# Kernel optimization log

Hardware: AMD Instinct MI355X
Metric: run time of the kernel (lower is better)

Reference implementation:

```python
import jax, jax.numpy as jnp
import numpy as np


def lstm_encode(x, Wih, Whh, b):
    """x: [S, T, F] -> final hidden state [S, H]. PyTorch LSTM gate order (i, f, g, o)."""
    S = x.shape[0]
    H = Whh.shape[1]

    def step(carry, xt):
        h, c = carry
        z = xt @ Wih.T + h @ Whh.T + b  # [S, 4H]
        i, f, g, o = jnp.split(z, 4, axis=-1)
        c = jax.nn.sigmoid(f) * c + jax.nn.sigmoid(i) * jnp.tanh(g)
        h = jax.nn.sigmoid(o) * jnp.tanh(c)
        return (h, c), None

    init = (jnp.zeros((S, H), x.dtype), jnp.zeros((S, H), x.dtype))
    (h, _), _ = jax.lax.scan(step, init, jnp.swapaxes(x, 0, 1))
    return h


def gatv2(h, Ws, Wd, a, bias):
    """Dense GATv2 on batched fully-connected graphs (no self loops).
    h: [G, N, Hin]; Ws, Wd: [nh, Hin, O]; a: [nh, O]; bias: [nh, O] -> [G, N, nh, O].
    Graph is fully connected (all i != j), so edge-softmax == dense row softmax
    with the diagonal masked out; this is the efficient dense form of the
    gather / LeakyReLU / edge-softmax / scatter pattern in DGL's GATv2Conv."""
    nh = Ws.shape[0]
    N = h.shape[1]
    self_mask = jnp.eye(N, dtype=bool)
    outs = []
    for hd in range(nh):  # small fixed head count; loop caps peak memory
        fs = h @ Ws[hd]  # [G, N, O] source-projected feats (messages)
        fd = h @ Wd[hd]  # [G, N, O] dst-projected feats
        e = jax.nn.leaky_relu(fd[:, :, None, :] + fs[:, None, :, :], 0.2)  # [G, dst, src, O]
        logits = jnp.where(self_mask, -jnp.inf, e @ a[hd])  # [G, dst, src]
        attn = jax.nn.softmax(logits, axis=-1)
        outs.append(jnp.einsum('gds,gso->gdo', attn, fs) + bias[hd])
    return jnp.stack(outs, axis=2)


def cosine(x, y, eps=1e-6):
    xn = x / jnp.maximum(jnp.linalg.norm(x, axis=-1, keepdims=True), eps)
    yn = y / jnp.maximum(jnp.linalg.norm(y, axis=-1, keepdims=True), eps)
    return (xn * yn).sum(-1)


def setup_inputs() -> dict:
    key = jax.random.key(0)
    B, K, T, N, F, H, GH, NH = 16, 4, 64, 128, 16, 32, 32, 8
    ks = jax.random.split(key, 16)

    def rn(k, shape, scale=1.0):
        return jax.random.normal(k, shape, jnp.float32) * scale

    return {
        'anchor': rn(ks[0], (B, T, N, F)),
        'pos': rn(ks[1], (B, T, N, F)),
        'neg': rn(ks[2], (B, K, T, N, F)),
        'hideout': rn(ks[3], (B, 2)),
        'timestep': jax.random.uniform(ks[4], (B, 1), jnp.float32),
        'Wih': rn(ks[5], (4 * H, F), 1.0 / np.sqrt(F)),
        'Whh': rn(ks[6], (4 * H, H), 1.0 / np.sqrt(H)),
        'b_lstm': rn(ks[7], (4 * H,), 0.1),
        'W1s': rn(ks[8], (NH, H, H), 1.0 / np.sqrt(H)),
        'W1d': rn(ks[9], (NH, H, H), 1.0 / np.sqrt(H)),
        'a1': rn(ks[10], (NH, H), 1.0 / np.sqrt(H)),
        'b1': rn(ks[11], (NH, H), 0.1),
        'W2s': rn(ks[12], (1, H, GH), 1.0 / np.sqrt(H)),
        'W2d': rn(ks[13], (1, H, GH), 1.0 / np.sqrt(H)),
        'a2': rn(ks[14], (1, GH), 1.0 / np.sqrt(GH)),
        'b2': rn(ks[15], (1, GH), 0.1),
        'num_agents': 128,
    }


def reference(anchor, pos, neg, hideout, timestep, Wih, Whh, b_lstm,
              W1s, W1d, a1, b1, W2s, W2d, a2, b2, num_agents):
    B, T, N, F = anchor.shape
    K = neg.shape[1]
    H = Whh.shape[1]
    # per-agent time series -> LSTM sequences
    a_seq = jnp.transpose(anchor, (0, 2, 1, 3)).reshape(B * N, T, F)
    p_seq = jnp.transpose(pos, (0, 2, 1, 3)).reshape(B * N, T, F)
    n_seq = jnp.transpose(neg, (0, 1, 3, 2, 4)).reshape(B * K * N, T, F)
    hn = lstm_encode(jnp.concatenate([a_seq, p_seq, n_seq], 0), Wih, Whh, b_lstm)
    hg = hn.reshape(-1, N, H)  # [(2+K)*B, N, H] batched fully-connected graphs
    h1 = gatv2(hg, W1s, W1d, a1, b1).mean(axis=2)  # mean over 8 heads
    h2 = gatv2(h1, W2s, W2d, a2, b2)[:, :, 0, :]   # single head, squeezed
    pooled = h2.mean(axis=1)                        # AvgPooling over nodes
    anchor_res = pooled[:B]
    pos_res = pooled[B:2 * B]
    neg_res = pooled[2 * B:].reshape(B, K, -1)
    sim_pos = cosine(anchor_res, pos_res)[:, None]      # [B, 1]
    sim_neg = cosine(anchor_res[:, None, :], neg_res)   # [B, K]
    all_vecs = jnp.concatenate([sim_neg, sim_pos], axis=1)  # positive last
    contrastive = (-jax.nn.log_softmax(all_vecs, axis=1)[:, -1]).mean()
    res = jnp.concatenate([anchor_res, hideout, timestep], axis=-1)
    return res, contrastive
```

## Files before the change

kernel.cpp:

```cpp
#include <hip/hip_runtime.h>
#include <math.h>


typedef __bf16 bf16x8 __attribute__((ext_vector_type(8)));
typedef float  f32x4  __attribute__((ext_vector_type(4)));
typedef unsigned int u32x4 __attribute__((ext_vector_type(4)));

__device__ __forceinline__ float fast_rcp(float x) { return __builtin_amdgcn_rcpf(x); }
__device__ __forceinline__ float sigm(float x)     { return fast_rcp(1.f + __expf(-x)); }
__device__ __forceinline__ float tanh_fast(float x){ return fmaf(2.f, fast_rcp(1.f + __expf(-2.f * x)), -1.f); }

#define KEEP4(x) asm volatile("" : "+v"(x))

__global__ __launch_bounds__(256, 1) void lstm_mfma_kernel(
    const float* __restrict__ anchor, const float* __restrict__ pos,
    const float* __restrict__ neg, const float* __restrict__ Wih,
    const float* __restrict__ Whh, const float* __restrict__ bias,
    float* __restrict__ hn)
{
    __shared__ unsigned int Hbuf[4][512];
    const int tid  = threadIdx.x;
    const int w    = tid >> 6;
    const int lane = tid & 63;
    const int l15  = lane & 15;
    const int g4   = lane >> 4;
    unsigned int* hb = Hbuf[w];

    #pragma unroll
    for (int i = 0; i < 8; ++i) hb[lane + i * 64] = 0u;

    u32x4 whhH[8], whhL[8], wihH[8];
    float bq[8];
    #pragma unroll
    for (int f = 0; f < 8; ++f) {
        const int G = f >> 1, Hh = f & 1;
        const int c = G * 32 + Hh * 16 + l15;
        bq[f] = bias[c];
        union { u32x4 u; bf16x8 v; } th, tl, ti;
        const float* wr = Whh + c * 32 + g4 * 8;
        #pragma unroll
        for (int i = 0; i < 8; ++i) {
            float wv = wr[i];
            __bf16 hi = (__bf16)wv;
            th.v[i] = hi;
            tl.v[i] = (__bf16)(wv - (float)hi);
        }
        if (g4 < 2) {
            const float* wr2 = Wih + c * 16 + g4 * 8;
            #pragma unroll
            for (int i = 0; i < 8; ++i) ti.v[i] = (__bf16)wr2[i];
        } else {
            #pragma unroll
            for (int i = 0; i < 8; ++i) ti.v[i] = (__bf16)0.f;
        }
        whhH[f] = th.u; whhL[f] = tl.u; wihH[f] = ti.u;
    }
    #pragma unroll
    for (int f = 0; f < 8; ++f) { KEEP4(whhH[f]); KEEP4(whhL[f]); KEEP4(wihH[f]); }

    const int s = blockIdx.x * 64 + w * 16 + l15;
    const float* xbase; int sl;
    if (s < 2048)      { xbase = anchor; sl = s; }
    else if (s < 4096) { xbase = pos;    sl = s - 2048; }
    else               { xbase = neg;    sl = s - 4096; }
    const bool xact = (g4 < 2);
    const float* xp = xbase + (sl >> 7) * 131072 + (sl & 127) * 16 + (xact ? g4 * 8 : 0);

    const float4 z4 = make_float4(0.f, 0.f, 0.f, 0.f);
    float4 xaA = z4, xbA = z4, xaB = z4, xbB = z4;
    if (xact) {
        xaA = *(const float4*)(xp);        xbA = *(const float4*)(xp + 4);
        xaB = *(const float4*)(xp + 2048); xbB = *(const float4*)(xp + 2052);
    }

    float cst[8] = {0.f,0.f,0.f,0.f,0.f,0.f,0.f,0.f};
    float hv[8]  = {0.f,0.f,0.f,0.f,0.f,0.f,0.f,0.f};

    #define LSTM_STEP(XA, XB)                                                          \
    {                                                                                  \
        bf16x8 ax;                                                                     \
        ax[0]=(__bf16)XA.x; ax[1]=(__bf16)XA.y; ax[2]=(__bf16)XA.z; ax[3]=(__bf16)XA.w;\
        ax[4]=(__bf16)XB.x; ax[5]=(__bf16)XB.y; ax[6]=(__bf16)XB.z; ax[7]=(__bf16)XB.w;\
        const int c0 = g4 * 2;                                                         \
        const int swz = (l15 & 3) << 1;                                                \
        uint4 v0 = *(const uint4*)(hb + l15 * 32 + ((c0 ^ swz) << 2));                 \
        uint4 v1 = *(const uint4*)(hb + l15 * 32 + (((c0 + 1) ^ swz) << 2));           \
        union { unsigned int u[4]; bf16x8 v; } ahi, alo;                               \
        ahi.u[0] = __builtin_amdgcn_perm(v0.y, v0.x, 0x05040100u);                     \
        ahi.u[1] = __builtin_amdgcn_perm(v0.w, v0.z, 0x05040100u);                     \
        ahi.u[2] = __builtin_amdgcn_perm(v1.y, v1.x, 0x05040100u);                     \
        ahi.u[3] = __builtin_amdgcn_perm(v1.w, v1.z, 0x05040100u);                     \
        alo.u[0] = __builtin_amdgcn_perm(v0.y, v0.x, 0x07060302u);                     \
        alo.u[1] = __builtin_amdgcn_perm(v0.w, v0.z, 0x07060302u);                     \
        alo.u[2] = __builtin_amdgcn_perm(v1.y, v1.x, 0x07060302u);                     \
        alo.u[3] = __builtin_amdgcn_perm(v1.w, v1.z, 0x07060302u);                     \
        f32x4 z[8];                                                                    \
        _Pragma("unroll")                                                              \
        for (int f = 0; f < 8; ++f) {                                                  \
            f32x4 a = __builtin_amdgcn_mfma_f32_16x16x32_bf16(                         \
                ax, __builtin_bit_cast(bf16x8, wihH[f]), (f32x4)(0.f), 0, 0, 0);       \
            a = __builtin_amdgcn_mfma_f32_16x16x32_bf16(                               \
                ahi.v, __builtin_bit_cast(bf16x8, whhH[f]), a, 0, 0, 0);               \
            a = __builtin_amdgcn_mfma_f32_16x16x32_bf16(                               \
                ahi.v, __builtin_bit_cast(bf16x8, whhL[f]), a, 0, 0, 0);               \
            a = __builtin_amdgcn_mfma_f32_16x16x32_bf16(                               \
                alo.v, __builtin_bit_cast(bf16x8, whhH[f]), a, 0, 0, 0);               \
            z[f] = a;                                                                  \
        }                                                                              \
        _Pragma("unroll")                                                              \
        for (int Hh = 0; Hh < 2; ++Hh) {                                               \
            _Pragma("unroll")                                                          \
            for (int r = 0; r < 4; ++r) {                                              \
                const int idx = Hh * 4 + r;                                            \
                float zi = z[0 + Hh][r] + bq[0 + Hh];                                  \
                float zf = z[2 + Hh][r] + bq[2 + Hh];                                  \
                float zg = z[4 + Hh][r] + bq[4 + Hh];                                  \
                float zo = z[6 + Hh][r] + bq[6 + Hh];                                  \
                float cn = fmaf(sigm(zf), cst[idx], sigm(zi) * tanh_fast(zg));         \
                cst[idx] = cn;                                                         \
                float h = sigm(zo) * tanh_fast(cn);                                    \
                hv[idx] = h;                                                           \
                __bf16 hh_ = (__bf16)h;                                                \
                __bf16 hl_ = (__bf16)(h - (float)hh_);                                 \
                unsigned int pk = (unsigned int)__builtin_bit_cast(unsigned short, hh_)\
                                | ((unsigned int)__builtin_bit_cast(unsigned short, hl_) << 16); \
                const int mm = g4 * 4 + r;                                             \
                const int jw = Hh * 16 + l15;                                          \
                hb[mm * 32 + (((jw >> 2) ^ ((mm & 3) << 1)) << 2) + (jw & 3)] = pk;    \
            }                                                                          \
        }                                                                              \
    }

    for (int t = 0; t < 64; t += 2) {
        float4 cA1 = xaA, cA2 = xbA;
        if (xact && t + 2 < 64) {
            const float* p = xp + (t + 2) * 2048;
            xaA = *(const float4*)(p); xbA = *(const float4*)(p + 4);
        }
        LSTM_STEP(cA1, cA2);

        float4 cB1 = xaB, cB2 = xbB;
        if (xact && t + 3 < 64) {
            const float* p = xp + (t + 3) * 2048;
            xaB = *(const float4*)(p); xbB = *(const float4*)(p + 4);
        }
        LSTM_STEP(cB1, cB2);
    }
    #undef LSTM_STEP

    const int seq0 = blockIdx.x * 64 + w * 16;
    #pragma unroll
    for (int Hh = 0; Hh < 2; ++Hh) {
        #pragma unroll
        for (int r = 0; r < 4; ++r) {
            hn[(seq0 + g4 * 4 + r) * 32 + Hh * 16 + l15] = hv[Hh * 4 + r];
        }
    }
}

__global__ __launch_bounds__(256) void gat1_kernel(
    const float* __restrict__ hn, const float* __restrict__ W1s,
    const float* __restrict__ W1d, const float* __restrict__ a1,
    const float* __restrict__ b1, float* __restrict__ h1heads)
{
    const int g = blockIdx.x >> 3, hd = blockIdx.x & 7;
    __shared__ float FS[128][36];
    __shared__ float FD[128][36];
    __shared__ float AVr[32];
    __shared__ float As06[128];
    __shared__ float Ad06[128];
    const int tid = threadIdx.x;

    if (tid < 32) AVr[tid] = a1[hd * 32 + tid];

    {
        const int o = tid & 31, nb = tid >> 5;
        float wcs[32], wcd[32];
        const float* wsp = W1s + hd * 1024 + o;
        const float* wdp = W1d + hd * 1024 + o;
        #pragma unroll
        for (int k = 0; k < 32; ++k) { wcs[k] = wsp[k * 32]; wcd[k] = wdp[k * 32]; }
        const float* hp = hn + g * 4096 + nb * 512;
        #pragma unroll 1
        for (int n = 0; n < 16; ++n) {
            float a0 = 0.f, a1_ = 0.f, b0 = 0.f, b1_ = 0.f;
            #pragma unroll
            for (int k0 = 0; k0 < 32; k0 += 4) {
                float4 hv = *(const float4*)(hp + n * 32 + k0);
                a0 = fmaf(hv.x, wcs[k0+0], a0); b0 = fmaf(hv.x, wcd[k0+0], b0);
                a1_ = fmaf(hv.y, wcs[k0+1], a1_); b1_ = fmaf(hv.y, wcd[k0+1], b1_);
                a0 = fmaf(hv.z, wcs[k0+2], a0); b0 = fmaf(hv.z, wcd[k0+2], b0);
                a1_ = fmaf(hv.w, wcs[k0+3], a1_); b1_ = fmaf(hv.w, wcd[k0+3], b1_);
            }
            FS[nb * 16 + n][o] = a0 + a1_;
            FD[nb * 16 + n][o] = b0 + b1_;
        }
    }
    __syncthreads();

    if (tid < 128) {
        float ss = 0.f, sd = 0.f;
        #pragma unroll
        for (int oo = 0; oo < 32; ++oo) {
            int o = (oo + tid) & 31;
            float a = AVr[o];
            ss = fmaf(a, FS[tid][o], ss);
            sd = fmaf(a, FD[tid][o], sd);
        }
        As06[tid] = 0.6f * ss;
        Ad06[tid] = 0.6f * sd;
    }
    __syncthreads();

    const int d = tid >> 1, sbase = (tid & 1) << 6;
    float fdr[32], avs[32];
    #pragma unroll
    for (int c = 0; c < 8; ++c) {
        float4 v = *(const float4*)&FD[d][c * 4];
        fdr[c*4+0] = v.x; fdr[c*4+1] = v.y; fdr[c*4+2] = v.z; fdr[c*4+3] = v.w;
        float4 w = *(const float4*)&AVr[c * 4];
        avs[c*4+0] = 0.4f * w.x; avs[c*4+1] = 0.4f * w.y;
        avs[c*4+2] = 0.4f * w.z; avs[c*4+3] = 0.4f * w.w;
    }
    const float adc = Ad06[d];

    float Z = 0.f;
    float acc[32];
    #pragma unroll
    for (int o = 0; o < 32; ++o) acc[o] = 0.f;
    #pragma unroll 1
    for (int si = 0; si < 64; ++si) {
        const int s = sbase + si;
        float4 fa[8];
        #pragma unroll
        for (int c = 0; c < 8; ++c) fa[c] = *(const float4*)&FS[s][c * 4];
        float c0 = 0.f, c1 = 0.f, c2 = 0.f, c3 = 0.f;
        #pragma unroll
        for (int c = 0; c < 8; ++c) {
            float e0 = fdr[c*4+0] + fa[c].x; c0 = fmaf(avs[c*4+0], __builtin_fabsf(e0), c0);
            float e1 = fdr[c*4+1] + fa[c].y; c1 = fmaf(avs[c*4+1], __builtin_fabsf(e1), c1);
            float e2 = fdr[c*4+2] + fa[c].z; c2 = fmaf(avs[c*4+2], __builtin_fabsf(e2), c2);
            float e3 = fdr[c*4+3] + fa[c].w; c3 = fmaf(avs[c*4+3], __builtin_fabsf(e3), c3);
        }
        float v = adc + As06[s] + ((c0 + c1) + (c2 + c3));
        float e = (s == d) ? 0.f : __expf(v);
        Z += e;
        #pragma unroll
        for (int c = 0; c < 8; ++c) {
            acc[c*4+0] = fmaf(e, fa[c].x, acc[c*4+0]);
            acc[c*4+1] = fmaf(e, fa[c].y, acc[c*4+1]);
            acc[c*4+2] = fmaf(e, fa[c].z, acc[c*4+2]);
            acc[c*4+3] = fmaf(e, fa[c].w, acc[c*4+3]);
        }
    }
    Z += __shfl_xor(Z, 1);
    const float rz = fast_rcp(Z);
    #pragma unroll
    for (int o = 0; o < 32; ++o) acc[o] += __shfl_xor(acc[o], 1);

    float* dst = h1heads + ((size_t)((g * 8 + hd) * 128 + d)) * 32;
    const float* bp = b1 + hd * 32;
    if ((tid & 1) == 0) {
        #pragma unroll
        for (int c = 0; c < 4; ++c) {
            float4 v;
            v.x = fmaf(acc[c*4+0], rz, bp[c*4+0]);
            v.y = fmaf(acc[c*4+1], rz, bp[c*4+1]);
            v.z = fmaf(acc[c*4+2], rz, bp[c*4+2]);
            v.w = fmaf(acc[c*4+3], rz, bp[c*4+3]);
            *(float4*)(dst + c * 4) = v;
        }
    } else {
        #pragma unroll
        for (int c = 4; c < 8; ++c) {
            float4 v;
            v.x = fmaf(acc[c*4+0], rz, bp[c*4+0]);
            v.y = fmaf(acc[c*4+1], rz, bp[c*4+1]);
            v.z = fmaf(acc[c*4+2], rz, bp[c*4+2]);
            v.w = fmaf(acc[c*4+3], rz, bp[c*4+3]);
            *(float4*)(dst + c * 4) = v;
        }
    }
}

__global__ __launch_bounds__(256) void gat2_kernel(
    const float* __restrict__ h1heads, const float* __restrict__ W2s,
    const float* __restrict__ W2d, const float* __restrict__ a2,
    const float* __restrict__ b2, float* __restrict__ pooled)
{
    const int g = blockIdx.x;
    __shared__ float HS[128][36];
    __shared__ float FS[128][36];
    __shared__ float FD[128][36];
    __shared__ float AVr[32];
    __shared__ float As06[128];
    __shared__ float Ad06[128];
    const int tid = threadIdx.x;

    if (tid < 32) AVr[tid] = a2[tid];

    {
        #pragma unroll
        for (int i = 0; i < 4; ++i) {
            int idx4 = i * 256 + tid;
            float sx = 0.f, sy = 0.f, sz = 0.f, sw = 0.f;
            #pragma unroll
            for (int hdd = 0; hdd < 8; ++hdd) {
                const float4* src = (const float4*)(h1heads + (size_t)(g * 8 + hdd) * 4096);
                float4 v = src[idx4];
                sx += v.x; sy += v.y; sz += v.z; sw += v.w;
            }
            int n = idx4 >> 3, k0 = (idx4 & 7) * 4;
            float4 r; r.x = sx * 0.125f; r.y = sy * 0.125f; r.z = sz * 0.125f; r.w = sw * 0.125f;
            *(float4*)&HS[n][k0] = r;
        }
    }
    __syncthreads();

    {
        const int o = tid & 31, nb = tid >> 5;
        float wcs[32], wcd[32];
        const float* wsp = W2s + o;
        const float* wdp = W2d + o;
        #pragma unroll
        for (int k = 0; k < 32; ++k) { wcs[k] = wsp[k * 32]; wcd[k] = wdp[k * 32]; }
        #pragma unroll 1
        for (int n = nb * 16; n < nb * 16 + 16; ++n) {
            float a0 = 0.f, a1_ = 0.f, b0 = 0.f, b1_ = 0.f;
            #pragma unroll
            for (int k0 = 0; k0 < 32; k0 += 4) {
                const float4 hv = *(const float4*)&HS[n][k0];
                a0 = fmaf(hv.x, wcs[k0+0], a0); b0 = fmaf(hv.x, wcd[k0+0], b0);
                a1_ = fmaf(hv.y, wcs[k0+1], a1_); b1_ = fmaf(hv.y, wcd[k0+1], b1_);
                a0 = fmaf(hv.z, wcs[k0+2], a0); b0 = fmaf(hv.z, wcd[k0+2], b0);
                a1_ = fmaf(hv.w, wcs[k0+3], a1_); b1_ = fmaf(hv.w, wcd[k0+3], b1_);
            }
            FS[n][o] = a0 + a1_;
            FD[n][o] = b0 + b1_;
        }
    }
    __syncthreads();

    if (tid < 128) {
        float ss = 0.f, sd = 0.f;
        #pragma unroll
        for (int oo = 0; oo < 32; ++oo) {
            int o = (oo + tid) & 31;
            float a = AVr[o];
            ss = fmaf(a, FS[tid][o], ss);
            sd = fmaf(a, FD[tid][o], sd);
        }
        As06[tid] = 0.6f * ss;
        Ad06[tid] = 0.6f * sd;
    }
    __syncthreads();

    const int d = tid >> 1, sbase = (tid & 1) << 6;
    float fdr[32], avs[32];
    #pragma unroll
    for (int c = 0; c < 8; ++c) {
        float4 v = *(const float4*)&FD[d][c * 4];
        fdr[c*4+0] = v.x; fdr[c*4+1] = v.y; fdr[c*4+2] = v.z; fdr[c*4+3] = v.w;
        float4 w = *(const float4*)&AVr[c * 4];
        avs[c*4+0] = 0.4f * w.x; avs[c*4+1] = 0.4f * w.y;
        avs[c*4+2] = 0.4f * w.z; avs[c*4+3] = 0.4f * w.w;
    }
    const float adc = Ad06[d];

    float Z = 0.f;
    float acc[32];
    #pragma unroll
    for (int o = 0; o < 32; ++o) acc[o] = 0.f;
    #pragma unroll 1
    for (int si = 0; si < 64; ++si) {
        const int s = sbase + si;
        float4 fa[8];
        #pragma unroll
        for (int c = 0; c < 8; ++c) fa[c] = *(const float4*)&FS[s][c * 4];
        float c0 = 0.f, c1 = 0.f, c2 = 0.f, c3 = 0.f;
        #pragma unroll
        for (int c = 0; c < 8; ++c) {
            float e0 = fdr[c*4+0] + fa[c].x; c0 = fmaf(avs[c*4+0], __builtin_fabsf(e0), c0);
            float e1 = fdr[c*4+1] + fa[c].y; c1 = fmaf(avs[c*4+1], __builtin_fabsf(e1), c1);
            float e2 = fdr[c*4+2] + fa[c].z; c2 = fmaf(avs[c*4+2], __builtin_fabsf(e2), c2);
            float e3 = fdr[c*4+3] + fa[c].w; c3 = fmaf(avs[c*4+3], __builtin_fabsf(e3), c3);
        }
        float v = adc + As06[s] + ((c0 + c1) + (c2 + c3));
        float e = (s == d) ? 0.f : __expf(v);
        Z += e;
        #pragma unroll
        for (int c = 0; c < 8; ++c) {
            acc[c*4+0] = fmaf(e, fa[c].x, acc[c*4+0]);
            acc[c*4+1] = fmaf(e, fa[c].y, acc[c*4+1]);
            acc[c*4+2] = fmaf(e, fa[c].z, acc[c*4+2]);
            acc[c*4+3] = fmaf(e, fa[c].w, acc[c*4+3]);
        }
    }
    Z += __shfl_xor(Z, 1);
    const float rz = fast_rcp(Z);
    #pragma unroll
    for (int o = 0; o < 32; ++o) acc[o] += __shfl_xor(acc[o], 1);

    __syncthreads();
    if ((tid & 1) == 0) {
        #pragma unroll
        for (int c = 0; c < 4; ++c) {
            float4 v;
            v.x = acc[c*4+0] * rz; v.y = acc[c*4+1] * rz;
            v.z = acc[c*4+2] * rz; v.w = acc[c*4+3] * rz;
            *(float4*)&FD[d][c * 4] = v;
        }
    } else {
        #pragma unroll
        for (int c = 4; c < 8; ++c) {
            float4 v;
            v.x = acc[c*4+0] * rz; v.y = acc[c*4+1] * rz;
            v.z = acc[c*4+2] * rz; v.w = acc[c*4+3] * rz;
            *(float4*)&FD[d][c * 4] = v;
        }
    }
    __syncthreads();

    if (tid < 32) {
        float sp = 0.f;
        #pragma unroll 1
        for (int n = 0; n < 128; ++n) sp += FD[n][tid];
        pooled[g * 32 + tid] = fmaf(sp, 1.f / 128.f, b2[tid]);
    }
}

__global__ void final_kernel(const float* __restrict__ pooled,
                             const float* __restrict__ hideout,
                             const float* __restrict__ timestep,
                             float* __restrict__ out)
{
    const int b = threadIdx.x;
    __shared__ float lossArr[16];
    if (b < 16) {
        const float* A  = pooled + b * 32;
        const float* Pv = pooled + (16 + b) * 32;
        float av[32];
        float na = 0.f;
        #pragma unroll
        for (int i = 0; i < 32; ++i) { av[i] = A[i]; na += av[i] * av[i]; }
        float npv = 0.f, dp = 0.f;
        #pragma unroll
        for (int i = 0; i < 32; ++i) { float p = Pv[i]; npv += p * p; dp += av[i] * p; }
        const float eps = 1e-6f;
        const float ia = 1.f / fmaxf(sqrtf(na), eps);
        const float sp = dp * ia / fmaxf(sqrtf(npv), eps);
        float sn[4];
        #pragma unroll
        for (int k = 0; k < 4; ++k) {
            const float* Nv = pooled + (32 + b * 4 + k) * 32;
            float nn = 0.f, dn = 0.f;
            #pragma unroll
            for (int i = 0; i < 32; ++i) { float q = Nv[i]; nn += q * q; dn += av[i] * q; }
            sn[k] = dn * ia / fmaxf(sqrtf(nn), eps);
        }
        float m = sp;
        #pragma unroll
        for (int k = 0; k < 4; ++k) m = fmaxf(m, sn[k]);
        float Z = expf(sp - m);
        #pragma unroll
        for (int k = 0; k < 4; ++k) Z += expf(sn[k] - m);
        lossArr[b] = logf(Z) + m - sp;
        float* r = out + b * 35;
        #pragma unroll
        for (int i = 0; i < 32; ++i) r[i] = av[i];
        r[32] = hideout[b * 2];
        r[33] = hideout[b * 2 + 1];
        r[34] = timestep[b];
    }
    __syncthreads();
    if (b == 0) {
        float s = 0.f;
        #pragma unroll
        for (int i = 0; i < 16; ++i) s += lossArr[i];
        out[560] = s * (1.f / 16.f);
    }
}

extern "C" void kernel_launch(void* const* d_in, const int* in_sizes, int n_in,
                              void* d_out, int out_size, void* d_ws, size_t ws_size,
                              hipStream_t stream) {
    const float* anchor   = (const float*)d_in[0];
    const float* pos      = (const float*)d_in[1];
    const float* neg      = (const float*)d_in[2];
    const float* hideout  = (const float*)d_in[3];
    const float* timestep = (const float*)d_in[4];
    const float* Wih      = (const float*)d_in[5];
    const float* Whh      = (const float*)d_in[6];
    const float* b_lstm   = (const float*)d_in[7];
    const float* W1s      = (const float*)d_in[8];
    const float* W1d      = (const float*)d_in[9];
    const float* a1       = (const float*)d_in[10];
    const float* b1       = (const float*)d_in[11];
    const float* W2s      = (const float*)d_in[12];
    const float* W2d      = (const float*)d_in[13];
    const float* a2       = (const float*)d_in[14];
    const float* b2       = (const float*)d_in[15];
    float* out = (float*)d_out;

    char* ws = (char*)d_ws;
    float* hn      = (float*)(ws);
    float* h1heads = (float*)(ws + 1605632);
    float* pooled  = (float*)(ws + 14188544);

    hipLaunchKernelGGL(lstm_mfma_kernel, dim3(192), dim3(256), 0, stream,
                       anchor, pos, neg, Wih, Whh, b_lstm, hn);
    hipLaunchKernelGGL(gat1_kernel,  dim3(768),  dim3(256), 0, stream,
                       hn, W1s, W1d, a1, b1, h1heads);
    hipLaunchKernelGGL(gat2_kernel,  dim3(96),   dim3(256), 0, stream,
                       h1heads, W2s, W2d, a2, b2, pooled);
    hipLaunchKernelGGL(final_kernel, dim3(1),    dim3(64),  0, stream,
                       pooled, hideout, timestep, out);
}
```

Measured before the change: 177.7 us.

## Drop LSTM hidden-state split precision and split GAT1 destinations across blocks

The LSTM recurrence stops storing the low-order bf16 residual of h and drops one of the four MFMAs per gate tile, which shortens the serial per-step chain at the cost of recurrent precision. GAT1 now splits each graph/head's destination nodes across two blocks (1536 blocks) with four threads per destination instead of two, raising parallelism but recomputing the source projections in both blocks. The FS shared array is also padded with a skew so row reads in both GAT kernels avoid bank conflicts.

```diff
diff --git a/kernel.cpp b/kernel.cpp
--- a/kernel.cpp
+++ b/kernel.cpp
@@ -73,27 +73,26 @@
         xaB = *(const float4*)(xp + 2048); xbB = *(const float4*)(xp + 2052);
     }
 
-    float cst[8] = {0.f,0.f,0.f,0.f,0.f,0.f,0.f,0.f};
-    float hv[8]  = {0.f,0.f,0.f,0.f,0.f,0.f,0.f,0.f};
+    float cst[8] = {0,0,0,0,0,0,0,0};
+    float hv[8]  = {0,0,0,0,0,0,0,0};
+
+    const int c0  = g4 * 2;
+    const int swz = (l15 & 3) << 1;
+    const int ro0 = l15 * 32 + ((c0 ^ swz) << 2);
+    const int ro1 = l15 * 32 + (((c0 + 1) ^ swz) << 2);
 
     #define LSTM_STEP(XA, XB)                                                          \
     {                                                                                  \
         bf16x8 ax;                                                                     \
         ax[0]=(__bf16)XA.x; ax[1]=(__bf16)XA.y; ax[2]=(__bf16)XA.z; ax[3]=(__bf16)XA.w;\
         ax[4]=(__bf16)XB.x; ax[5]=(__bf16)XB.y; ax[6]=(__bf16)XB.z; ax[7]=(__bf16)XB.w;\
-        const int c0 = g4 * 2;                                                         \
-        const int swz = (l15 & 3) << 1;                                                \
-        uint4 v0 = *(const uint4*)(hb + l15 * 32 + ((c0 ^ swz) << 2));                 \
-        uint4 v1 = *(const uint4*)(hb + l15 * 32 + (((c0 + 1) ^ swz) << 2));           \
-        union { unsigned int u[4]; bf16x8 v; } ahi, alo;                               \
+        uint4 v0 = *(const uint4*)(hb + ro0);                                          \
+        uint4 v1 = *(const uint4*)(hb + ro1);                                          \
+        union { unsigned int u[4]; bf16x8 v; } ahi;                                    \
         ahi.u[0] = __builtin_amdgcn_perm(v0.y, v0.x, 0x05040100u);                     \
         ahi.u[1] = __builtin_amdgcn_perm(v0.w, v0.z, 0x05040100u);                     \
         ahi.u[2] = __builtin_amdgcn_perm(v1.y, v1.x, 0x05040100u);                     \
         ahi.u[3] = __builtin_amdgcn_perm(v1.w, v1.z, 0x05040100u);                     \
-        alo.u[0] = __builtin_amdgcn_perm(v0.y, v0.x, 0x07060302u);                     \
-        alo.u[1] = __builtin_amdgcn_perm(v0.w, v0.z, 0x07060302u);                     \
-        alo.u[2] = __builtin_amdgcn_perm(v1.y, v1.x, 0x07060302u);                     \
-        alo.u[3] = __builtin_amdgcn_perm(v1.w, v1.z, 0x07060302u);                     \
         f32x4 z[8];                                                                    \
         _Pragma("unroll")                                                              \
         for (int f = 0; f < 8; ++f) {                                                  \
@@ -103,8 +102,6 @@
                 ahi.v, __builtin_bit_cast(bf16x8, whhH[f]), a, 0, 0, 0);               \
             a = __builtin_amdgcn_mfma_f32_16x16x32_bf16(                               \
                 ahi.v, __builtin_bit_cast(bf16x8, whhL[f]), a, 0, 0, 0);               \
-            a = __builtin_amdgcn_mfma_f32_16x16x32_bf16(                               \
-                alo.v, __builtin_bit_cast(bf16x8, whhH[f]), a, 0, 0, 0);               \
             z[f] = a;                                                                  \
         }                                                                              \
         _Pragma("unroll")                                                              \
@@ -120,10 +117,8 @@
                 cst[idx] = cn;                                                         \
                 float h = sigm(zo) * tanh_fast(cn);                                    \
                 hv[idx] = h;                                                           \
-                __bf16 hh_ = (__bf16)h;                                                \
-                __bf16 hl_ = (__bf16)(h - (float)hh_);                                 \
-                unsigned int pk = (unsigned int)__builtin_bit_cast(unsigned short, hh_)\
-                                | ((unsigned int)__builtin_bit_cast(unsigned short, hl_) << 16); \
+                unsigned int pk = (unsigned int)__builtin_bit_cast(unsigned short,     \
+                                                                   (__bf16)h);        \
                 const int mm = g4 * 4 + r;                                             \
                 const int jw = Hh * 16 + l15;                                          \
                 hb[mm * 32 + (((jw >> 2) ^ ((mm & 3) << 1)) << 2) + (jw & 3)] = pk;    \
@@ -158,17 +153,20 @@
     }
 }
 
+__device__ __forceinline__ int fsoff(int n) { return n * 36 + ((n >> 5) << 2); }
+
 __global__ __launch_bounds__(256) void gat1_kernel(
     const float* __restrict__ hn, const float* __restrict__ W1s,
     const float* __restrict__ W1d, const float* __restrict__ a1,
     const float* __restrict__ b1, float* __restrict__ h1heads)
 {
-    const int g = blockIdx.x >> 3, hd = blockIdx.x & 7;
-    __shared__ float FS[128][36];
-    __shared__ float FD[128][36];
+    const int g = blockIdx.x >> 4, hd = (blockIdx.x >> 1) & 7, half = blockIdx.x & 1;
+    const int dbase = half << 6;
+    __shared__ float FSf[128 * 36 + 16];
+    __shared__ float FD[64][36];
     __shared__ float AVr[32];
     __shared__ float As06[128];
-    __shared__ float Ad06[128];
+    __shared__ float Ad06[64];
     const int tid = threadIdx.x;
 
     if (tid < 32) AVr[tid] = a1[hd * 32 + tid];
@@ -181,8 +179,10 @@
         #pragma unroll
         for (int k = 0; k < 32; ++k) { wcs[k] = wsp[k * 32]; wcd[k] = wdp[k * 32]; }
         const float* hp = hn + g * 4096 + nb * 512;
+        const bool own = (nb >> 2) == half;
         #pragma unroll 1
         for (int n = 0; n < 16; ++n) {
+            const int row = nb * 16 + n;
             float a0 = 0.f, a1_ = 0.f, b0 = 0.f, b1_ = 0.f;
             #pragma unroll
             for (int k0 = 0; k0 < 32; k0 += 4) {
@@ -192,48 +192,56 @@
                 a0 = fmaf(hv.z, wcs[k0+2], a0); b0 = fmaf(hv.z, wcd[k0+2], b0);
                 a1_ = fmaf(hv.w, wcs[k0+3], a1_); b1_ = fmaf(hv.w, wcd[k0+3], b1_);
             }
-            FS[nb * 16 + n][o] = a0 + a1_;
-            FD[nb * 16 + n][o] = b0 + b1_;
+            FSf[fsoff(row) + o] = a0 + a1_;
+            if (own) FD[row - dbase][o] = b0 + b1_;
         }
     }
     __syncthreads();
 
     if (tid < 128) {
-        float ss = 0.f, sd = 0.f;
+        float ss = 0.f;
+        const float* fr = FSf + fsoff(tid);
         #pragma unroll
         for (int oo = 0; oo < 32; ++oo) {
             int o = (oo + tid) & 31;
-            float a = AVr[o];
-            ss = fmaf(a, FS[tid][o], ss);
-            sd = fmaf(a, FD[tid][o], sd);
+            ss = fmaf(AVr[o], fr[o], ss);
         }
         As06[tid] = 0.6f * ss;
-        Ad06[tid] = 0.6f * sd;
-    }
-    __syncthreads();
-
-    const int d = tid >> 1, sbase = (tid & 1) << 6;
+    } else if (tid < 192) {
+        const int dl = tid - 128;
+        float sd = 0.f;
+        #pragma unroll
+        for (int oo = 0; oo < 32; ++oo) {
+            int o = (oo + dl) & 31;
+            sd = fmaf(AVr[o], FD[dl][o], sd);
+        }
+        Ad06[dl] = 0.6f * sd;
+    }
+    __syncthreads();
+
+    const int dl = tid >> 2, d = dbase + dl, sq = tid & 3, sbase = sq << 5;
     float fdr[32], avs[32];
     #pragma unroll
     for (int c = 0; c < 8; ++c) {
-        float4 v = *(const float4*)&FD[d][c * 4];
+        float4 v = *(const float4*)&FD[dl][c * 4];
         fdr[c*4+0] = v.x; fdr[c*4+1] = v.y; fdr[c*4+2] = v.z; fdr[c*4+3] = v.w;
-        float4 w = *(const float4*)&AVr[c * 4];
-        avs[c*4+0] = 0.4f * w.x; avs[c*4+1] = 0.4f * w.y;
-        avs[c*4+2] = 0.4f * w.z; avs[c*4+3] = 0.4f * w.w;
-    }
-    const float adc = Ad06[d];
+        float4 wv = *(const float4*)&AVr[c * 4];
+        avs[c*4+0] = 0.4f * wv.x; avs[c*4+1] = 0.4f * wv.y;
+        avs[c*4+2] = 0.4f * wv.z; avs[c*4+3] = 0.4f * wv.w;
+    }
+    const float adc = Ad06[dl];
 
     float Z = 0.f;
     float acc[32];
     #pragma unroll
     for (int o = 0; o < 32; ++o) acc[o] = 0.f;
     #pragma unroll 1
-    for (int si = 0; si < 64; ++si) {
+    for (int si = 0; si < 32; ++si) {
         const int s = sbase + si;
+        const float* fr = FSf + fsoff(s);
         float4 fa[8];
         #pragma unroll
-        for (int c = 0; c < 8; ++c) fa[c] = *(const float4*)&FS[s][c * 4];
+        for (int c = 0; c < 8; ++c) fa[c] = *(const float4*)(fr + c * 4);
         float c0 = 0.f, c1 = 0.f, c2 = 0.f, c3 = 0.f;
         #pragma unroll
         for (int c = 0; c < 8; ++c) {
@@ -253,26 +261,19 @@
             acc[c*4+3] = fmaf(e, fa[c].w, acc[c*4+3]);
         }
     }
-    Z += __shfl_xor(Z, 1);
+    Z += __shfl_xor(Z, 1); Z += __shfl_xor(Z, 2);
     const float rz = fast_rcp(Z);
     #pragma unroll
-    for (int o = 0; o < 32; ++o) acc[o] += __shfl_xor(acc[o], 1);
-
-    float* dst = h1heads + ((size_t)((g * 8 + hd) * 128 + d)) * 32;
-    const float* bp = b1 + hd * 32;
-    if ((tid & 1) == 0) {
-        #pragma unroll
-        for (int c = 0; c < 4; ++c) {
-            float4 v;
-            v.x = fmaf(acc[c*4+0], rz, bp[c*4+0]);
-            v.y = fmaf(acc[c*4+1], rz, bp[c*4+1]);
-            v.z = fmaf(acc[c*4+2], rz, bp[c*4+2]);
-            v.w = fmaf(acc[c*4+3], rz, bp[c*4+3]);
-            *(float4*)(dst + c * 4) = v;
-        }
-    } else {
-        #pragma unroll
-        for (int c = 4; c < 8; ++c) {
+    for (int o = 0; o < 32; ++o) {
+        acc[o] += __shfl_xor(acc[o], 1);
+        acc[o] += __shfl_xor(acc[o], 2);
+    }
+
+    if (sq == 0) {
+        float* dst = h1heads + ((size_t)((g * 8 + hd) * 128 + d)) * 32;
+        const float* bp = b1 + hd * 32;
+        #pragma unroll
+        for (int c = 0; c < 8; ++c) {
             float4 v;
             v.x = fmaf(acc[c*4+0], rz, bp[c*4+0]);
             v.y = fmaf(acc[c*4+1], rz, bp[c*4+1]);
@@ -290,7 +291,7 @@
 {
     const int g = blockIdx.x;
     __shared__ float HS[128][36];
-    __shared__ float FS[128][36];
+    __shared__ float FSf[128 * 36 + 16];
     __shared__ float FD[128][36];
     __shared__ float AVr[32];
     __shared__ float As06[128];
@@ -335,7 +336,7 @@
                 a0 = fmaf(hv.z, wcs[k0+2], a0); b0 = fmaf(hv.z, wcd[k0+2], b0);
                 a1_ = fmaf(hv.w, wcs[k0+3], a1_); b1_ = fmaf(hv.w, wcd[k0+3], b1_);
             }
-            FS[n][o] = a0 + a1_;
+            FSf[fsoff(n) + o] = a0 + a1_;
             FD[n][o] = b0 + b1_;
         }
     }
@@ -343,11 +344,12 @@
 
     if (tid < 128) {
         float ss = 0.f, sd = 0.f;
+        const float* fr = FSf + fsoff(tid);
         #pragma unroll
         for (int oo = 0; oo < 32; ++oo) {
             int o = (oo + tid) & 31;
             float a = AVr[o];
-            ss = fmaf(a, FS[tid][o], ss);
+            ss = fmaf(a, fr[o], ss);
             sd = fmaf(a, FD[tid][o], sd);
         }
         As06[tid] = 0.6f * ss;
@@ -361,9 +363,9 @@
     for (int c = 0; c < 8; ++c) {
         float4 v = *(const float4*)&FD[d][c * 4];
         fdr[c*4+0] = v.x; fdr[c*4+1] = v.y; fdr[c*4+2] = v.z; fdr[c*4+3] = v.w;
-        float4 w = *(const float4*)&AVr[c * 4];
-        avs[c*4+0] = 0.4f * w.x; avs[c*4+1] = 0.4f * w.y;
-        avs[c*4+2] = 0.4f * w.z; avs[c*4+3] = 0.4f * w.w;
+        float4 wv = *(const float4*)&AVr[c * 4];
+        avs[c*4+0] = 0.4f * wv.x; avs[c*4+1] = 0.4f * wv.y;
+        avs[c*4+2] = 0.4f * wv.z; avs[c*4+3] = 0.4f * wv.w;
     }
     const float adc = Ad06[d];
 
@@ -374,9 +376,10 @@
     #pragma unroll 1
     for (int si = 0; si < 64; ++si) {
         const int s = sbase + si;
+        const float* fr = FSf + fsoff(s);
         float4 fa[8];
         #pragma unroll
-        for (int c = 0; c < 8; ++c) fa[c] = *(const float4*)&FS[s][c * 4];
+        for (int c = 0; c < 8; ++c) fa[c] = *(const float4*)(fr + c * 4);
         float c0 = 0.f, c1 = 0.f, c2 = 0.f, c3 = 0.f;
         #pragma unroll
         for (int c = 0; c < 8; ++c) {
@@ -509,7 +512,7 @@
 
     hipLaunchKernelGGL(lstm_mfma_kernel, dim3(192), dim3(256), 0, stream,
                        anchor, pos, neg, Wih, Whh, b_lstm, hn);
-    hipLaunchKernelGGL(gat1_kernel,  dim3(768),  dim3(256), 0, stream,
+    hipLaunchKernelGGL(gat1_kernel,  dim3(1536), dim3(256), 0, stream,
                        hn, W1s, W1d, a1, b1, h1heads);
     hipLaunchKernelGGL(gat2_kernel,  dim3(96),   dim3(256), 0, stream,
                        h1heads, W2s, W2d, a2, b2, pooled);
```

After: 166.5 us. -6.3%, faster.
